# Kernel optimization log

Measured on AMD Instinct MI355X. Metric: run time of the kernel, lower is better.

The kernel has to match this reference:

```python
import jax, jax.numpy as jnp
import numpy as np

N, E, G, H = 4096, 8192, 64, 128  # nodes, edges, graphs, hidden dim
NODE_DIM, EDGE_DIM = 11, 5


def _linear_params(key, fan_in, fan_out):
    kw, kb = jax.random.split(key)
    s = 1.0 / np.sqrt(fan_in)
    w = jax.random.uniform(kw, (fan_in, fan_out), minval=-s, maxval=s, dtype=jnp.float32)
    b = jax.random.uniform(kb, (fan_out,), minval=-s, maxval=s, dtype=jnp.float32)
    return w, b


def setup_inputs() -> dict:
    key = jax.random.key(0)
    ks = jax.random.split(key, 10)
    x = jax.random.normal(ks[0], (N, NODE_DIM), dtype=jnp.float32)
    edge_attr = jax.random.normal(ks[1], (E, EDGE_DIM), dtype=jnp.float32)
    edge_index = jax.random.randint(ks[2], (2, E), 0, N, dtype=jnp.int64)
    batch = jnp.sort(jax.random.randint(ks[3], (N,), 0, G, dtype=jnp.int64))
    # preprocess MLP: node_dim -> 128 -> 128
    p1_w, p1_b = _linear_params(ks[4], NODE_DIM, H)
    p2_w, p2_b = _linear_params(ks[5], H, H)
    # edge net: edge_dim -> 128 -> 256 -> 128 -> 128*128 (ReLU between, none after last)
    e1_w, e1_b = _linear_params(ks[6], EDGE_DIM, 128)
    e2_w, e2_b = _linear_params(ks[7], 128, 256)
    e3_w, e3_b = _linear_params(ks[8], 256, 128)
    e4_w, e4_b = _linear_params(ks[9], 128, H * H)
    return {"x": x, "edge_attr": edge_attr, "edge_index": edge_index, "batch": batch,
            "p1_w": p1_w, "p1_b": p1_b, "p2_w": p2_w, "p2_b": p2_b,
            "e1_w": e1_w, "e1_b": e1_b, "e2_w": e2_w, "e2_b": e2_b,
            "e3_w": e3_w, "e3_b": e3_b, "e4_w": e4_w, "e4_b": e4_b}


def reference(x, edge_attr, edge_index, batch,
              p1_w, p1_b, p2_w, p2_b,
              e1_w, e1_b, e2_w, e2_b, e3_w, e3_b, e4_w, e4_b):
    # node preprocess MLP (maps 11-dim features to 128 so NNConv dims are consistent)
    h = jax.nn.relu(x @ p1_w + p1_b) @ p2_w + p2_b  # [N, H]
    # edge network -> per-edge weight matrix [E, H, H]
    e = jax.nn.relu(edge_attr @ e1_w + e1_b)
    e = jax.nn.relu(e @ e2_w + e2_b)
    e = jax.nn.relu(e @ e3_w + e3_b)
    W = (e @ e4_w + e4_b).reshape(E, H, H)
    # NNConv (root_weight=False, bias=False, aggr='mean'):
    src, dst = edge_index[0], edge_index[1]
    msg = jnp.einsum('ei,eio->eo', h[src], W)  # gather + per-edge matmul, [E, H]
    agg = jax.ops.segment_sum(msg, dst, num_segments=N)
    cnt = jax.ops.segment_sum(jnp.ones((E,), msg.dtype), dst, num_segments=N)
    h_out = agg / jnp.maximum(cnt, 1.0)[:, None]  # scatter-mean, [N, H]
    # global add pool over graphs
    pooled = jax.ops.segment_sum(h_out, batch, num_segments=G)  # [G, H]
    return pooled
```

## Files before the change

### kernel.cpp

```cpp
#include <hip/hip_runtime.h>
#include <hip/hip_bf16.h>

#define N_NODES 4096
#define N_EDGES 8192
#define N_GRAPHS 64
#define HDIM 128

typedef __attribute__((ext_vector_type(8))) short bf16x8;
typedef __attribute__((ext_vector_type(4))) float f32x4;

static __device__ __forceinline__ unsigned short f2bf(float f) {
    unsigned u = __builtin_bit_cast(unsigned, f);
    u += 0x7fffu + ((u >> 16) & 1u);
    return (unsigned short)(u >> 16);
}
static __device__ __forceinline__ float bf2f(unsigned short s) {
    unsigned u = ((unsigned)s) << 16;
    return __builtin_bit_cast(float, u);
}

__global__ __launch_bounds__(256) void fused_pre_edge_kernel(
    const float* __restrict__ x, const float* __restrict__ p1w, const float* __restrict__ p1b,
    const float* __restrict__ p2w, const float* __restrict__ p2b, const float* __restrict__ e4b,
    unsigned short* __restrict__ h_bf, float* __restrict__ hb,
    const float* __restrict__ ea, const float* __restrict__ w1, const float* __restrict__ b1,
    const float* __restrict__ w2, const float* __restrict__ b2,
    const float* __restrict__ w3, const float* __restrict__ b3,
    unsigned short* __restrict__ e3bf,
    const float* __restrict__ w4, unsigned short* __restrict__ w4perm,
    float* __restrict__ aggz)
{
    __shared__ __align__(16) char smem[33024];
    const int t = threadIdx.x;
    const int bid = blockIdx.x;

    if (bid < 512) {
        float (*es)[5] = (float(*)[5])smem;
        unsigned short* l1a = (unsigned short*)(smem + 320);
        unsigned short* l2a = (unsigned short*)(smem + 4672);
        const int w = t >> 6, lane = t & 63, q = lane >> 4, l15 = lane & 15;
        const int e0 = bid * 16;
        const f32x4 zero4 = (f32x4){0.f, 0.f, 0.f, 0.f};

        for (int r = t; r < 80; r += 256) es[r / 5][r % 5] = ea[e0 * 5 + r];
        __syncthreads();
        {
            int j = t & 127, eh = t >> 7;
            float wd[5];
            #pragma unroll
            for (int d = 0; d < 5; ++d) wd[d] = w1[d * 128 + j];
            float bj = b1[j];
            #pragma unroll
            for (int p = 0; p < 8; ++p) {
                int e = eh * 8 + p;
                float acc = bj;
                #pragma unroll
                for (int d = 0; d < 5; ++d) acc += es[e][d] * wd[d];
                l1a[e * 136 + j] = f2bf(fmaxf(acc, 0.f));
            }
        }
        __syncthreads();

        bf16x8 afrag[4];
        #pragma unroll
        for (int s = 0; s < 4; ++s)
            afrag[s] = *(const bf16x8*)&l1a[l15 * 136 + s * 32 + q * 8];

        f32x4 acc[4];
        #pragma unroll
        for (int ob = 0; ob < 4; ++ob) acc[ob] = zero4;
        #pragma unroll
        for (int ob = 0; ob < 4; ++ob) {
            const int o = w * 64 + ob * 16 + l15;
            bf16x8 bfrag[4];
            #pragma unroll
            for (int s = 0; s < 4; ++s) {
                const int kb = s * 32 + q * 8;
                #pragma unroll
                for (int kk = 0; kk < 8; ++kk)
                    bfrag[s][kk] = (short)f2bf(w2[(kb + kk) * 256 + o]);
            }
            f32x4 tmp = __builtin_amdgcn_mfma_f32_16x16x32_bf16(afrag[0], bfrag[0], zero4, 0, 0, 0);
            tmp = __builtin_amdgcn_mfma_f32_16x16x32_bf16(afrag[1], bfrag[1], tmp, 0, 0, 0);
            tmp = __builtin_amdgcn_mfma_f32_16x16x32_bf16(afrag[2], bfrag[2], tmp, 0, 0, 0);
            acc[ob] = __builtin_amdgcn_mfma_f32_16x16x32_bf16(afrag[3], bfrag[3], tmp, 0, 0, 0);
        }
        #pragma unroll
        for (int ob = 0; ob < 4; ++ob) {
            int o = w * 64 + ob * 16 + l15;
            float bo = b2[o];
            #pragma unroll
            for (int r = 0; r < 4; ++r) {
                int e_loc = q * 4 + r;
                l2a[e_loc * 264 + o] = f2bf(fmaxf(acc[ob][r] + bo, 0.f));
            }
        }
        __syncthreads();

        f32x4 acc3[2];
        acc3[0] = zero4; acc3[1] = zero4;
        #pragma unroll
        for (int ks = 0; ks < 8; ++ks) {
            bf16x8 a3 = *(const bf16x8*)&l2a[l15 * 264 + ks * 32 + q * 8];
            #pragma unroll
            for (int ob = 0; ob < 2; ++ob) {
                const int o = w * 32 + ob * 16 + l15;
                bf16x8 bf;
                const int kb = ks * 32 + q * 8;
                #pragma unroll
                for (int kk = 0; kk < 8; ++kk)
                    bf[kk] = (short)f2bf(w3[(kb + kk) * 128 + o]);
                acc3[ob] = __builtin_amdgcn_mfma_f32_16x16x32_bf16(a3, bf, acc3[ob], 0, 0, 0);
            }
        }
        #pragma unroll
        for (int ob = 0; ob < 2; ++ob) {
            int o = w * 32 + ob * 16 + l15;
            float bo = b3[o];
            #pragma unroll
            for (int r = 0; r < 4; ++r) {
                int e = e0 + q * 4 + r;
                e3bf[(size_t)e * 128 + o] = f2bf(fmaxf(acc3[ob][r] + bo, 0.f));
            }
        }
    } else if (bid < 768) {
        float (*xs)[11]  = (float(*)[11])smem;
        float (*l1t)[16] = (float(*)[16])(smem + 704);
        float (*hs)[16]  = (float(*)[16])(smem + 8896);
        const int nb = bid - 512;

        for (int r = t; r < 16 * 11; r += 256) {
            int e = r / 11, d = r % 11;
            xs[e][d] = x[(nb * 16 + e) * 11 + d];
        }
        __syncthreads();
        {
            int j = t & 127;
            float wd[11];
            #pragma unroll
            for (int d = 0; d < 11; ++d) wd[d] = p1w[d * 128 + j];
            float bj = p1b[j];
            for (int p = 0; p < 8; ++p) {
                int e = p * 2 + (t >> 7);
                float acc = bj;
                #pragma unroll
                for (int d = 0; d < 11; ++d) acc += xs[e][d] * wd[d];
                l1t[j][e] = fmaxf(acc, 0.f);
            }
        }
        __syncthreads();
        {
            int j = t & 127, eh = t >> 7;
            float acc[8];
            float bj = p2b[j];
            #pragma unroll
            for (int r = 0; r < 8; ++r) acc[r] = bj;
            #pragma unroll 8
            for (int k = 0; k < 128; ++k) {
                float w = p2w[k * 128 + j];
                const float4* row = (const float4*)&l1t[k][eh * 8];
                float4 v0 = row[0], v1 = row[1];
                acc[0] += v0.x * w; acc[1] += v0.y * w; acc[2] += v0.z * w; acc[3] += v0.w * w;
                acc[4] += v1.x * w; acc[5] += v1.y * w; acc[6] += v1.z * w; acc[7] += v1.w * w;
            }
            #pragma unroll
            for (int r = 0; r < 8; ++r) {
                int e = eh * 8 + r;
                h_bf[(nb * 16 + e) * 128 + j] = f2bf(acc[r]);
                hs[j][e] = acc[r];
            }
        }
        __syncthreads();
        {
            int j = t & 127, eh = t >> 7;
            float acc[8] = {0.f,0.f,0.f,0.f,0.f,0.f,0.f,0.f};
            #pragma unroll 8
            for (int i = 0; i < 128; ++i) {
                float w = e4b[i * 128 + j];
                const float4* row = (const float4*)&hs[i][eh * 8];
                float4 v0 = row[0], v1 = row[1];
                acc[0] += v0.x * w; acc[1] += v0.y * w; acc[2] += v0.z * w; acc[3] += v0.w * w;
                acc[4] += v1.x * w; acc[5] += v1.y * w; acc[6] += v1.z * w; acc[7] += v1.w * w;
            }
            #pragma unroll
            for (int r = 0; r < 8; ++r) hb[(nb * 16 + eh * 8 + r) * 128 + j] = acc[r];
        }
    } else if (bid < 896) {
        unsigned short (*tt)[129] = (unsigned short(*)[129])smem;
        const int i = bid - 768;
        for (int r = t; r < 16384; r += 256) {
            int k = r >> 7, o = r & 127;
            tt[o][k] = f2bf(w4[k * 16384 + i * 128 + o]);
        }
        __syncthreads();
        for (int r = t; r < 16384; r += 256) {
            int o = r >> 7, k = r & 127;
            w4perm[((size_t)(o >> 5) * 128 + i) * 4352 + (size_t)(o & 31) * 136 + k] = tt[o][k];
        }
    } else {
        float4* dst = (float4*)aggz;
        const float4 z = make_float4(0.f, 0.f, 0.f, 0.f);
        for (int i = (bid - 896) * 256 + t; i < 132096; i += 128 * 256) dst[i] = z;
    }
}

__global__ __launch_bounds__(256, 3) void nnconv_kernel(
    const unsigned short* __restrict__ e3bf, const unsigned short* __restrict__ h_bf,
    const unsigned short* __restrict__ w4perm, const float* __restrict__ hb,
    const int* __restrict__ ei, float* __restrict__ agg, float* __restrict__ cnt)
{
    __shared__ __align__(16) float ht_f[64 * 64];
    __shared__ __align__(16) float red[2 * 64 * 16];
    const int t = threadIdx.x;
    const int bid = blockIdx.x;
    const int osplit = bid & 3;
    const int ksplit = (bid >> 2) & 1;
    const int etile  = bid >> 3;
    const int w = t >> 6, lane = t & 63, q = lane >> 4, l15 = lane & 15;
    const int og   = w & 1;
    const int kpar = w >> 1;
    const int e0 = etile * 64;
    const int o0 = osplit * 32;
    const int i0 = ksplit * 64;

    bf16x8 afrag[4][4];
    #pragma unroll
    for (int mb = 0; mb < 4; ++mb)
        #pragma unroll
        for (int s = 0; s < 4; ++s) {
            int row = e0 + mb * 16 + l15;
            afrag[mb][s] = *(const bf16x8*)(e3bf + (size_t)row * 128 + s * 32 + q * 8);
        }
    #pragma unroll
    for (int mb = 0; mb < 4; ++mb)
        #pragma unroll
        for (int s = 0; s < 4; ++s)
            asm volatile("" : "+v"(afrag[mb][s]));
    asm volatile("" ::: "memory");

    {
        int r = t >> 2, part = t & 3;
        int s = ei[e0 + r];
        #pragma unroll
        for (int u = 0; u < 2; ++u) {
            uint4 v = *(const uint4*)(h_bf + (size_t)s * 128 + i0 + part * 16 + u * 8);
            const unsigned short* pv = (const unsigned short*)&v;
            #pragma unroll
            for (int j = 0; j < 8; ++j)
                ht_f[(part * 16 + u * 8 + j) * 64 + r] = bf2f(pv[j]);
        }
    }

    f32x4 acc[4];
    #pragma unroll
    for (int mb = 0; mb < 4; ++mb) acc[mb] = (f32x4){0.f, 0.f, 0.f, 0.f};
    const f32x4 zero4 = (f32x4){0.f, 0.f, 0.f, 0.f};

    __syncthreads();

    const unsigned short* bbase =
        w4perm + ((size_t)osplit * 128 + i0 + kpar * 32) * 4352
               + (size_t)(og * 16 + l15) * 136 + q * 8;
    #pragma unroll 2
    for (int c = 0; c < 32; ++c) {
        const unsigned short* bp = bbase + (size_t)c * 4352;
        bf16x8 bfrag[4];
        #pragma unroll
        for (int s = 0; s < 4; ++s)
            bfrag[s] = *(const bf16x8*)(bp + s * 32);
        const int cg = kpar * 32 + c;
        #pragma unroll
        for (int mb = 0; mb < 4; ++mb) {
            f32x4 hv = *(const f32x4*)&ht_f[cg * 64 + mb * 16 + q * 4];
            f32x4 tmp = __builtin_amdgcn_mfma_f32_16x16x32_bf16(afrag[mb][0], bfrag[0], zero4, 0, 0, 0);
            tmp = __builtin_amdgcn_mfma_f32_16x16x32_bf16(afrag[mb][1], bfrag[1], tmp, 0, 0, 0);
            tmp = __builtin_amdgcn_mfma_f32_16x16x32_bf16(afrag[mb][2], bfrag[2], tmp, 0, 0, 0);
            tmp = __builtin_amdgcn_mfma_f32_16x16x32_bf16(afrag[mb][3], bfrag[3], tmp, 0, 0, 0);
            #pragma unroll
            for (int r = 0; r < 4; ++r)
                acc[mb][r] += hv[r] * tmp[r];
        }
    }

    if (kpar == 1) {
        #pragma unroll
        for (int mb = 0; mb < 4; ++mb)
            #pragma unroll
            for (int r = 0; r < 4; ++r)
                red[(og * 64 + mb * 16 + q * 4 + r) * 16 + l15] = acc[mb][r];
    }
    __syncthreads();
    if (kpar == 0) {
        #pragma unroll
        for (int mb = 0; mb < 4; ++mb) {
            #pragma unroll
            for (int r = 0; r < 4; ++r) {
                int e_loc = mb * 16 + q * 4 + r;
                int e = e0 + e_loc;
                int de = ei[N_EDGES + e];
                int se = ei[e];
                int o = o0 + og * 16 + l15;
                float v = acc[mb][r] + red[(og * 64 + e_loc) * 16 + l15];
                if (ksplit == 0) v += hb[(size_t)se * 128 + o];
                if (osplit == 0 && ksplit == 0 && og == 0 && l15 == 0)
                    atomicAdd(&cnt[de], 1.0f);
                atomicAdd(&agg[(size_t)de * 128 + o], v);
            }
        }
    }
}

__global__ __launch_bounds__(512) void pool_kernel(
    const float* __restrict__ agg, const float* __restrict__ cnt,
    const int* __restrict__ batch, float* __restrict__ out)
{
    __shared__ float ps[4][128];
    const int g = blockIdx.x;
    const int ch = threadIdx.x & 127, th = threadIdx.x >> 7;
    int lo = 0, hi = N_NODES;
    while (lo < hi) { int m = (lo + hi) >> 1; if (batch[m] < g) lo = m + 1; else hi = m; }
    const int n_lo = lo;
    int lo2 = n_lo, hi2 = N_NODES;
    while (lo2 < hi2) { int m = (lo2 + hi2) >> 1; if (batch[m] < g + 1) lo2 = m + 1; else hi2 = m; }
    const int n_hi = lo2;

    float s = 0.f;
    for (int n = n_lo + th; n < n_hi; n += 4) {
        float c = cnt[n];
        c = c > 1.f ? c : 1.f;
        s += agg[n * 128 + ch] / c;
    }
    ps[th][ch] = s;
    __syncthreads();
    if (th == 0)
        out[g * 128 + ch] = (ps[0][ch] + ps[1][ch]) + (ps[2][ch] + ps[3][ch]);
}

extern "C" void kernel_launch(void* const* d_in, const int* in_sizes, int n_in,
                              void* d_out, int out_size, void* d_ws, size_t ws_size,
                              hipStream_t stream)
{
    const float* x     = (const float*)d_in[0];
    const float* ea    = (const float*)d_in[1];
    const int*   ei    = (const int*)d_in[2];
    const int*   batch = (const int*)d_in[3];
    const float* p1w   = (const float*)d_in[4];
    const float* p1b   = (const float*)d_in[5];
    const float* p2w   = (const float*)d_in[6];
    const float* p2b   = (const float*)d_in[7];
    const float* w1    = (const float*)d_in[8];
    const float* b1    = (const float*)d_in[9];
    const float* w2    = (const float*)d_in[10];
    const float* b2    = (const float*)d_in[11];
    const float* w3    = (const float*)d_in[12];
    const float* b3    = (const float*)d_in[13];
    const float* w4    = (const float*)d_in[14];
    const float* b4    = (const float*)d_in[15];
    float* out = (float*)d_out;
    (void)in_sizes; (void)n_in; (void)out_size; (void)ws_size;

    char* ws = (char*)d_ws;
    unsigned short* h_bf = (unsigned short*)(ws);
    unsigned short* e3bf = (unsigned short*)(ws + 1048576);
    float* hb            = (float*)(ws + 3145728);
    unsigned short* w4p  = (unsigned short*)(ws + 5242880);
    float* agg           = (float*)(ws + 9699328);
    float* cnt           = (float*)(ws + 11796480);

    fused_pre_edge_kernel<<<1024, 256, 0, stream>>>(
        x, p1w, p1b, p2w, p2b, b4, h_bf, hb,
        ea, w1, b1, w2, b2, w3, b3, e3bf,
        w4, w4p, agg);
    nnconv_kernel<<<1024, 256, 0, stream>>>(e3bf, h_bf, w4p, hb, ei, agg, cnt);
    pool_kernel<<<N_GRAPHS, 512, 0, stream>>>(agg, cnt, batch, out);
}
```

Before: 169.5 us.

## Stage W4 tiles into LDS with async multi-buffered global_load_lds pipeline

The NNConv kernel now streams the permuted W4 slices through a 4-deep LDS ring using direct global-to-LDS loads, waiting on vmcnt and a barrier before each MFMA step, instead of having each wave load B fragments from global memory. Each block covers 128 edges across two wave row-groups that share B tiles, so the intra-block k-split reduction through shared memory goes away and the grid is halved. The W4 layout drops its 136-element padding and uses an XOR swizzle to avoid LDS bank conflicts, and MFMA sections run at raised wave priority. In exchange LDS use and register pressure rise, occupancy drops to 2 blocks per CU, and the hand-counted vmcnt waits must stay in step with the staged loads.

```diff
diff --git a/kernel.cpp b/kernel.cpp
--- a/kernel.cpp
+++ b/kernel.cpp
@@ -195,7 +195,8 @@
         __syncthreads();
         for (int r = t; r < 16384; r += 256) {
             int o = r >> 7, k = r & 127;
-            w4perm[((size_t)(o >> 5) * 128 + i) * 4352 + (size_t)(o & 31) * 136 + k] = tt[o][k];
+            w4perm[((size_t)(o >> 5) * 128 + i) * 4096
+                   + (size_t)(o & 31) * 128 + (k ^ ((o & 7) << 3))] = tt[o][k];
         }
     } else {
         float4* dst = (float4*)aggz;
@@ -204,31 +205,48 @@
     }
 }
 
-__global__ __launch_bounds__(256, 3) void nnconv_kernel(
+__global__ __launch_bounds__(256, 2) void nnconv_kernel(
     const unsigned short* __restrict__ e3bf, const unsigned short* __restrict__ h_bf,
     const unsigned short* __restrict__ w4perm, const float* __restrict__ hb,
     const int* __restrict__ ei, float* __restrict__ agg, float* __restrict__ cnt)
 {
-    __shared__ __align__(16) float ht_f[64 * 64];
-    __shared__ __align__(16) float red[2 * 64 * 16];
+    __shared__ __align__(16) float ht_f[64 * 128];
+    __shared__ __align__(16) unsigned short ldsB[4 * 4096];
     const int t = threadIdx.x;
     const int bid = blockIdx.x;
-    const int osplit = bid & 3;
-    const int ksplit = (bid >> 2) & 1;
+    const int xcd    = bid & 7;
+    const int osplit = xcd >> 1;
+    const int ksplit = xcd & 1;
     const int etile  = bid >> 3;
     const int w = t >> 6, lane = t & 63, q = lane >> 4, l15 = lane & 15;
-    const int og   = w & 1;
-    const int kpar = w >> 1;
-    const int e0 = etile * 64;
+    const int mg = w >> 1;
+    const int og = w & 1;
+    const int e0 = etile * 128;
     const int o0 = osplit * 32;
-    const int i0 = ksplit * 64;
+    const int k0 = ksplit * 64;
+    const int oloc = og * 16 + l15;
+    const int oswz = (oloc & 7) << 3;
+
+    auto stage = [&](int buf, int gi) {
+        const char* src = (const char*)(w4perm + ((size_t)osplit * 128 + gi) * 4096);
+        char* dst = (char*)ldsB + buf * 8192;
+        __builtin_amdgcn_global_load_lds(
+            (const __attribute__((address_space(1))) unsigned int*)(src + t * 16),
+            (__attribute__((address_space(3))) unsigned int*)(dst + t * 16), 16, 0, 0);
+        __builtin_amdgcn_global_load_lds(
+            (const __attribute__((address_space(1))) unsigned int*)(src + 4096 + t * 16),
+            (__attribute__((address_space(3))) unsigned int*)(dst + 4096 + t * 16), 16, 0, 0);
+    };
+
+    stage(0, k0);
+    stage(1, k0 + 1);
 
     bf16x8 afrag[4][4];
     #pragma unroll
     for (int mb = 0; mb < 4; ++mb)
         #pragma unroll
         for (int s = 0; s < 4; ++s) {
-            int row = e0 + mb * 16 + l15;
+            int row = e0 + mg * 64 + mb * 16 + l15;
             afrag[mb][s] = *(const bf16x8*)(e3bf + (size_t)row * 128 + s * 32 + q * 8);
         }
     #pragma unroll
@@ -239,15 +257,15 @@
     asm volatile("" ::: "memory");
 
     {
-        int r = t >> 2, part = t & 3;
+        int r = t >> 1, part = t & 1;
         int s = ei[e0 + r];
         #pragma unroll
-        for (int u = 0; u < 2; ++u) {
-            uint4 v = *(const uint4*)(h_bf + (size_t)s * 128 + i0 + part * 16 + u * 8);
+        for (int u = 0; u < 4; ++u) {
+            uint4 v = *(const uint4*)(h_bf + (size_t)s * 128 + k0 + part * 32 + u * 8);
             const unsigned short* pv = (const unsigned short*)&v;
             #pragma unroll
             for (int j = 0; j < 8; ++j)
-                ht_f[(part * 16 + u * 8 + j) * 64 + r] = bf2f(pv[j]);
+                ht_f[(part * 32 + u * 8 + j) * 128 + r] = bf2f(pv[j]);
         }
     }
 
@@ -258,20 +276,17 @@
 
     __syncthreads();
 
-    const unsigned short* bbase =
-        w4perm + ((size_t)osplit * 128 + i0 + kpar * 32) * 4352
-               + (size_t)(og * 16 + l15) * 136 + q * 8;
-    #pragma unroll 2
-    for (int c = 0; c < 32; ++c) {
-        const unsigned short* bp = bbase + (size_t)c * 4352;
+    auto compute = [&](int bufu16, int ci) {
         bf16x8 bfrag[4];
         #pragma unroll
-        for (int s = 0; s < 4; ++s)
-            bfrag[s] = *(const bf16x8*)(bp + s * 32);
-        const int cg = kpar * 32 + c;
+        for (int s = 0; s < 4; ++s) {
+            int kb = s * 32 + q * 8;
+            bfrag[s] = *(const bf16x8*)&ldsB[bufu16 + oloc * 128 + (kb ^ oswz)];
+        }
+        __builtin_amdgcn_s_setprio(1);
         #pragma unroll
         for (int mb = 0; mb < 4; ++mb) {
-            f32x4 hv = *(const f32x4*)&ht_f[cg * 64 + mb * 16 + q * 4];
+            f32x4 hv = *(const f32x4*)&ht_f[ci * 128 + mg * 64 + mb * 16 + q * 4];
             f32x4 tmp = __builtin_amdgcn_mfma_f32_16x16x32_bf16(afrag[mb][0], bfrag[0], zero4, 0, 0, 0);
             tmp = __builtin_amdgcn_mfma_f32_16x16x32_bf16(afrag[mb][1], bfrag[1], tmp, 0, 0, 0);
             tmp = __builtin_amdgcn_mfma_f32_16x16x32_bf16(afrag[mb][2], bfrag[2], tmp, 0, 0, 0);
@@ -280,32 +295,34 @@
             for (int r = 0; r < 4; ++r)
                 acc[mb][r] += hv[r] * tmp[r];
         }
-    }
-
-    if (kpar == 1) {
-        #pragma unroll
-        for (int mb = 0; mb < 4; ++mb)
-            #pragma unroll
-            for (int r = 0; r < 4; ++r)
-                red[(og * 64 + mb * 16 + q * 4 + r) * 16 + l15] = acc[mb][r];
-    }
-    __syncthreads();
-    if (kpar == 0) {
-        #pragma unroll
-        for (int mb = 0; mb < 4; ++mb) {
-            #pragma unroll
-            for (int r = 0; r < 4; ++r) {
-                int e_loc = mb * 16 + q * 4 + r;
-                int e = e0 + e_loc;
-                int de = ei[N_EDGES + e];
-                int se = ei[e];
-                int o = o0 + og * 16 + l15;
-                float v = acc[mb][r] + red[(og * 64 + e_loc) * 16 + l15];
-                if (ksplit == 0) v += hb[(size_t)se * 128 + o];
-                if (osplit == 0 && ksplit == 0 && og == 0 && l15 == 0)
-                    atomicAdd(&cnt[de], 1.0f);
-                atomicAdd(&agg[(size_t)de * 128 + o], v);
-            }
+        __builtin_amdgcn_s_setprio(0);
+    };
+
+    for (int c = 0; c < 62; ++c) {
+        stage((c + 2) & 3, k0 + c + 2);
+        asm volatile("s_waitcnt vmcnt(4)" ::: "memory");
+        __builtin_amdgcn_s_barrier();
+        compute((c & 3) * 4096, c);
+    }
+    asm volatile("s_waitcnt vmcnt(2)" ::: "memory");
+    __builtin_amdgcn_s_barrier();
+    compute((62 & 3) * 4096, 62);
+    asm volatile("s_waitcnt vmcnt(0)" ::: "memory");
+    __builtin_amdgcn_s_barrier();
+    compute((63 & 3) * 4096, 63);
+
+    #pragma unroll
+    for (int mb = 0; mb < 4; ++mb) {
+        #pragma unroll
+        for (int r = 0; r < 4; ++r) {
+            int e = e0 + mg * 64 + mb * 16 + q * 4 + r;
+            int de = ei[N_EDGES + e];
+            int se = ei[e];
+            int o = o0 + oloc;
+            float v = acc[mb][r];
+            if (ksplit == 0) v += hb[(size_t)se * 128 + o];
+            if (xcd == 0 && og == 0 && l15 == 0) atomicAdd(&cnt[de], 1.0f);
+            atomicAdd(&agg[(size_t)de * 128 + o], v);
         }
     }
 }
@@ -371,6 +388,6 @@
         x, p1w, p1b, p2w, p2b, b4, h_bf, hb,
         ea, w1, b1, w2, b2, w3, b3, e3bf,
         w4, w4p, agg);
-    nnconv_kernel<<<1024, 256, 0, stream>>>(e3bf, h_bf, w4p, hb, ei, agg, cnt);
+    nnconv_kernel<<<512, 256, 0, stream>>>(e3bf, h_bf, w4p, hb, ei, agg, cnt);
     pool_kernel<<<N_GRAPHS, 512, 0, stream>>>(agg, cnt, batch, out);
 }
```

After: 175.6 us. +3.6%, slower.
